# Kernel optimization log

Hardware: AMD Instinct MI355X
Metric: run time of the kernel (lower is better)

## Reference

```python
import jax, jax.numpy as jnp
from jax import lax
import numpy as np

H, W, C = 2160, 3840, 3
CROP = 3  # rows trimmed top and bottom before filtering


def median1d(x, size, axis):
    """Sliding-window median along `axis` with edge padding (matches
    np.pad(mode='edge') + centered window + np.median for odd size)."""
    pad = size // 2
    pw = [(0, 0)] * x.ndim
    pw[axis] = (pad, pad)
    xp = jnp.pad(x, pw, mode='edge')
    n = x.shape[axis]
    # stack the `size` shifted views -> (..., size), median = middle of sort
    windows = jnp.stack(
        [lax.slice_in_dim(xp, i, i + n, axis=axis) for i in range(size)], axis=-1)
    return jnp.sort(windows, axis=-1)[..., size // 2]


def shift1(x, axis):
    """np.pad(x,(1,0),'constant')[:-1] along `axis`: shift forward, zero-fill."""
    pw = [(0, 0)] * x.ndim
    pw[axis] = (1, 0)
    return lax.slice_in_dim(jnp.pad(x, pw), 0, x.shape[axis], axis=axis)


def setup_inputs() -> dict:
    key = jax.random.key(0)
    k1, k2 = jax.random.split(key)
    img = jax.random.normal(k1, (H, W, C), dtype=jnp.float32)
    mask = jax.random.randint(k2, (H, W), 0, 2, dtype=jnp.int32)
    return {"img": img, "mask": mask, "vertical_size": 5}


def reference(img, mask, vertical_size):
    # mask is read but unused by the original module's math.
    x = img[CROP:-CROP]                       # (H-6, W, C)
    # vertical pass: median(v), shift down 1, median(3) along rows
    v = median1d(x, vertical_size, axis=0)
    v = median1d(shift1(v, axis=0), 3, axis=0)
    # horizontal pass (original reuses vertical_size here): along columns
    h = median1d(v, vertical_size, axis=1)
    h = median1d(shift1(h, axis=1), 3, axis=1)
    return h
```

## Files before the change

### kernel.cpp

```cpp
#include <hip/hip_runtime.h>

#define HH    2160
#define WW    3840
#define CROPC 3
#define NN    (HH - 2*CROPC)
#define WFLAT (WW * 3)

constexpr int TY    = 16;
constexpr int TXF   = 192;
constexpr int SX    = TXF + 18;
constexpr int NTH   = 256;
constexpr int TPR   = 16;
constexpr int XROWS = TY + 6;

constexpr int PSTR  = 76;
constexpr int PLANE = TY * PSTR + 8;

__device__ __forceinline__ float vmed3(float a, float b, float c) {
    float r;
    asm("v_med3_f32 %0, %1, %2, %3" : "=v"(r) : "v"(a), "v"(b), "v"(c));
    return r;
}

__global__ __launch_bounds__(NTH, 8) void fused_median(const float* __restrict__ img,
                                                       float* __restrict__ out) {
    __shared__ float v2s[3 * PLANE];

    const int tid = threadIdx.x;
    const int r0 = blockIdx.y * TY;
    const int f0 = blockIdx.x * TXF;

    if (tid < SX) {
        const int ch   = tid % 3;
        const int pcol = tid / 3;
        const int cc   = min(max(f0 / 3 - 4 + pcol, 0), WW - 1);
        const float* colp = img + (size_t)CROPC * WFLAT + (cc * 3 + ch);

        float xv[XROWS];
        #pragma unroll
        for (int i = 0; i < XROWS; ++i) {
            const int rr = min(max(r0 - 4 + i, 0), NN - 1);
            xv[i] = colp[(size_t)rr * WFLAT];
        }
        asm volatile("" ::
            "v"(xv[0]),  "v"(xv[1]),  "v"(xv[2]),  "v"(xv[3]),  "v"(xv[4]),
            "v"(xv[5]),  "v"(xv[6]),  "v"(xv[7]),  "v"(xv[8]),  "v"(xv[9]),
            "v"(xv[10]), "v"(xv[11]), "v"(xv[12]), "v"(xv[13]), "v"(xv[14]),
            "v"(xv[15]), "v"(xv[16]), "v"(xv[17]), "v"(xv[18]), "v"(xv[19]),
            "v"(xv[20]), "v"(xv[21]));

        float lo0 = fminf(xv[0], xv[1]), hi0 = fmaxf(xv[0], xv[1]);
        float lo1 = fminf(xv[1], xv[2]), hi1 = fmaxf(xv[1], xv[2]);
        float vm2 = 0.f, vm1 = 0.f;
        #pragma unroll
        for (int s = 0; s < 18; ++s) {
            const float lo2 = fminf(xv[s+2], xv[s+3]);
            const float hi2 = fmaxf(xv[s+2], xv[s+3]);
            const float vc  = vmed3(xv[s+4], fmaxf(lo0, lo2), fminf(hi0, hi2));
            if (s >= 2) {
                const int rz = r0 + s - 2;
                float a = vm2, b = vm1;
                if (rz == NN - 1) a = b;
                if (rz == 1)      a = 0.f;
                if (rz == 0)    { a = 0.f; b = 0.f; }
                v2s[ch * PLANE + (s - 2) * PSTR + pcol] = vmed3(a, b, vc);
            }
            lo0 = lo1; hi0 = hi1; lo1 = lo2; hi1 = hi2;
            vm2 = vm1; vm1 = vc;
        }
    }
    __syncthreads();

    const int lr    = tid >> 4;
    const int kk    = tid & (TPR - 1);
    const int r_out = r0 + lr;
    if (r_out >= NN) return;

    const int cbase = f0 / 3 + 4 * kk;
    const bool edge = (cbase <= 1) || (cbase + 3 >= WW - 1);

    float o[12];
    #pragma unroll
    for (int c = 0; c < 3; ++c) {
        const float* pb = &v2s[c * PLANE + lr * PSTR + 4 * kk];
        const float4 q0 = *(const float4*)(pb);
        const float4 q1 = *(const float4*)(pb + 4);
        const float2 q2 = *(const float2*)(pb + 8);
        const float ss[10] = {q0.x,q0.y,q0.z,q0.w, q1.x,q1.y,q1.z,q1.w,
                              q2.x,q2.y};
        float plo[8], phi[8];
        #pragma unroll
        for (int i = 0; i < 8; ++i) {
            plo[i] = fminf(ss[i], ss[i+1]);
            phi[i] = fmaxf(ss[i], ss[i+1]);
        }
        float h[6];
        #pragma unroll
        for (int m = 0; m < 6; ++m)
            h[m] = vmed3(ss[m+4], fmaxf(plo[m], plo[m+2]), fminf(phi[m], phi[m+2]));
        if (!edge) {
            #pragma unroll
            for (int n = 0; n < 4; ++n)
                o[3*n + c] = vmed3(h[n], h[n+1], h[n+2]);
        } else {
            #pragma unroll
            for (int n = 0; n < 4; ++n) {
                const int ci = cbase + n;
                float A = h[n], B = h[n+1];
                if (ci == WW - 1) A = B;
                if (ci == 1)      A = 0.f;
                if (ci == 0)    { A = 0.f; B = 0.f; }
                o[3*n + c] = vmed3(A, B, h[n+2]);
            }
        }
    }

    float4* op = (float4*)(out + (size_t)r_out * WFLAT + f0 + 12 * kk);
    op[0] = make_float4(o[0], o[1], o[2],  o[3]);
    op[1] = make_float4(o[4], o[5], o[6],  o[7]);
    op[2] = make_float4(o[8], o[9], o[10], o[11]);
}

extern "C" void kernel_launch(void* const* d_in, const int* in_sizes, int n_in,
                              void* d_out, int out_size, void* d_ws, size_t ws_size,
                              hipStream_t stream) {
    const float* img = (const float*)d_in[0];
    float* out = (float*)d_out;
    dim3 grid(WFLAT / TXF, (NN + TY - 1) / TY);
    fused_median<<<grid, NTH, 0, stream>>>(img, out);
}
```

Before: 48.65 us.

## Replace shared-memory horizontal pass with wavefront shuffles, dropping the block barrier

The horizontal median passes now exchange neighbouring columns through cross-lane shuffles within each 64-lane wavefront, replacing the LDS staging buffer and the __syncthreads. Each wavefront computes 46 output floats and loads 18 halo lanes, so every thread does the vertical pass. Stores become scalar per-lane writes instead of float4 vectors. In exchange, about 28% of loaded columns are redundant halo, each row costs six shuffles, and stores are narrower.

```diff
diff --git a/kernel.cpp b/kernel.cpp
--- a/kernel.cpp
+++ b/kernel.cpp
@@ -7,118 +7,90 @@
 #define WFLAT (WW * 3)
 
 constexpr int TY    = 16;
-constexpr int TXF   = 192;
-constexpr int SX    = TXF + 18;
-constexpr int NTH   = 256;
-constexpr int TPR   = 16;
+constexpr int OPW   = 46;
+constexpr int WPB   = 4;
+constexpr int NTH   = 64 * WPB;
+constexpr int OPB   = OPW * WPB;
 constexpr int XROWS = TY + 6;
-
-constexpr int PSTR  = 76;
-constexpr int PLANE = TY * PSTR + 8;
 
 __device__ __forceinline__ float vmed3(float a, float b, float c) {
     float r;
     asm("v_med3_f32 %0, %1, %2, %3" : "=v"(r) : "v"(a), "v"(b), "v"(c));
     return r;
 }
+__device__ __forceinline__ float med5_7(float a, float b, float c, float d, float e) {
+    const float lo1 = fminf(a, b), hi1 = fmaxf(a, b);
+    const float lo2 = fminf(c, d), hi2 = fmaxf(c, d);
+    return vmed3(e, fmaxf(lo1, lo2), fminf(hi1, hi2));
+}
 
 __global__ __launch_bounds__(NTH, 8) void fused_median(const float* __restrict__ img,
                                                        float* __restrict__ out) {
-    __shared__ float v2s[3 * PLANE];
+    const int tid  = threadIdx.x;
+    const int lane = tid & 63;
+    const int wv   = tid >> 6;
+    const int r0   = blockIdx.y * TY;
+    const int fp12 = blockIdx.x * OPB + wv * OPW + lane;
+    const int fl   = fp12 - 12;
+    const int ch   = fp12 % 3;
+    const int cc   = min(max(fp12 / 3 - 4, 0), WW - 1);
+    const float* colp = img + (size_t)CROPC * WFLAT + (cc * 3 + ch);
 
-    const int tid = threadIdx.x;
-    const int r0 = blockIdx.y * TY;
-    const int f0 = blockIdx.x * TXF;
+    const int  ci       = fl / 3;
+    const bool store_ok = (lane >= 12) && (lane < 58) && (fl < WFLAT);
 
-    if (tid < SX) {
-        const int ch   = tid % 3;
-        const int pcol = tid / 3;
-        const int cc   = min(max(f0 / 3 - 4 + pcol, 0), WW - 1);
-        const float* colp = img + (size_t)CROPC * WFLAT + (cc * 3 + ch);
+    const int lm6 = max(lane - 6, 0), lm3 = max(lane - 3, 0);
+    const int lp3 = min(lane + 3, 63), lp6 = min(lane + 6, 63);
 
-        float xv[XROWS];
-        #pragma unroll
-        for (int i = 0; i < XROWS; ++i) {
-            const int rr = min(max(r0 - 4 + i, 0), NN - 1);
-            xv[i] = colp[(size_t)rr * WFLAT];
+    float xv[XROWS];
+    #pragma unroll
+    for (int i = 0; i < XROWS; ++i) {
+        const int rr = min(max(r0 - 4 + i, 0), NN - 1);
+        xv[i] = colp[(size_t)rr * WFLAT];
+    }
+    asm volatile("" ::
+        "v"(xv[0]),  "v"(xv[1]),  "v"(xv[2]),  "v"(xv[3]),  "v"(xv[4]),
+        "v"(xv[5]),  "v"(xv[6]),  "v"(xv[7]),  "v"(xv[8]),  "v"(xv[9]),
+        "v"(xv[10]), "v"(xv[11]), "v"(xv[12]), "v"(xv[13]), "v"(xv[14]),
+        "v"(xv[15]), "v"(xv[16]), "v"(xv[17]), "v"(xv[18]), "v"(xv[19]),
+        "v"(xv[20]), "v"(xv[21]));
+
+    float lo0 = fminf(xv[0], xv[1]), hi0 = fmaxf(xv[0], xv[1]);
+    float lo1 = fminf(xv[1], xv[2]), hi1 = fmaxf(xv[1], xv[2]);
+    float vm2 = 0.f, vm1 = 0.f;
+    #pragma unroll
+    for (int s = 0; s < TY + 2; ++s) {
+        const float lo2 = fminf(xv[s+2], xv[s+3]);
+        const float hi2 = fmaxf(xv[s+2], xv[s+3]);
+        const float vc  = vmed3(xv[s+4], fmaxf(lo0, lo2), fminf(hi0, hi2));
+        if (s >= 2) {
+            const int rz = r0 + s - 2;
+            float a = vm2, b = vm1;
+            if (rz == NN - 1) a = b;
+            if (rz == 1)      a = 0.f;
+            if (rz == 0)    { a = 0.f; b = 0.f; }
+            const float w = vmed3(a, b, vc);
+
+            const float m6 = __shfl(w, lm6, 64);
+            const float m3 = __shfl(w, lm3, 64);
+            const float p3 = __shfl(w, lp3, 64);
+            const float p6 = __shfl(w, lp6, 64);
+            const float h0 = med5_7(m6, m3, p3, p6, w);
+
+            const float hm3 = __shfl(h0, lm3, 64);
+            const float hm6 = __shfl(h0, lm6, 64);
+            float A = hm6, B = hm3;
+            if (ci == WW - 1) A = B;
+            if (ci == 1)      A = 0.f;
+            if (ci == 0)    { A = 0.f; B = 0.f; }
+            const float o = vmed3(A, B, h0);
+
+            if (store_ok && rz < NN)
+                out[(size_t)rz * WFLAT + fl] = o;
         }
-        asm volatile("" ::
-            "v"(xv[0]),  "v"(xv[1]),  "v"(xv[2]),  "v"(xv[3]),  "v"(xv[4]),
-            "v"(xv[5]),  "v"(xv[6]),  "v"(xv[7]),  "v"(xv[8]),  "v"(xv[9]),
-            "v"(xv[10]), "v"(xv[11]), "v"(xv[12]), "v"(xv[13]), "v"(xv[14]),
-            "v"(xv[15]), "v"(xv[16]), "v"(xv[17]), "v"(xv[18]), "v"(xv[19]),
-            "v"(xv[20]), "v"(xv[21]));
-
-        float lo0 = fminf(xv[0], xv[1]), hi0 = fmaxf(xv[0], xv[1]);
-        float lo1 = fminf(xv[1], xv[2]), hi1 = fmaxf(xv[1], xv[2]);
-        float vm2 = 0.f, vm1 = 0.f;
-        #pragma unroll
-        for (int s = 0; s < 18; ++s) {
-            const float lo2 = fminf(xv[s+2], xv[s+3]);
-            const float hi2 = fmaxf(xv[s+2], xv[s+3]);
-            const float vc  = vmed3(xv[s+4], fmaxf(lo0, lo2), fminf(hi0, hi2));
-            if (s >= 2) {
-                const int rz = r0 + s - 2;
-                float a = vm2, b = vm1;
-                if (rz == NN - 1) a = b;
-                if (rz == 1)      a = 0.f;
-                if (rz == 0)    { a = 0.f; b = 0.f; }
-                v2s[ch * PLANE + (s - 2) * PSTR + pcol] = vmed3(a, b, vc);
-            }
-            lo0 = lo1; hi0 = hi1; lo1 = lo2; hi1 = hi2;
-            vm2 = vm1; vm1 = vc;
-        }
+        lo0 = lo1; hi0 = hi1; lo1 = lo2; hi1 = hi2;
+        vm2 = vm1; vm1 = vc;
     }
-    __syncthreads();
-
-    const int lr    = tid >> 4;
-    const int kk    = tid & (TPR - 1);
-    const int r_out = r0 + lr;
-    if (r_out >= NN) return;
-
-    const int cbase = f0 / 3 + 4 * kk;
-    const bool edge = (cbase <= 1) || (cbase + 3 >= WW - 1);
-
-    float o[12];
-    #pragma unroll
-    for (int c = 0; c < 3; ++c) {
-        const float* pb = &v2s[c * PLANE + lr * PSTR + 4 * kk];
-        const float4 q0 = *(const float4*)(pb);
-        const float4 q1 = *(const float4*)(pb + 4);
-        const float2 q2 = *(const float2*)(pb + 8);
-        const float ss[10] = {q0.x,q0.y,q0.z,q0.w, q1.x,q1.y,q1.z,q1.w,
-                              q2.x,q2.y};
-        float plo[8], phi[8];
-        #pragma unroll
-        for (int i = 0; i < 8; ++i) {
-            plo[i] = fminf(ss[i], ss[i+1]);
-            phi[i] = fmaxf(ss[i], ss[i+1]);
-        }
-        float h[6];
-        #pragma unroll
-        for (int m = 0; m < 6; ++m)
-            h[m] = vmed3(ss[m+4], fmaxf(plo[m], plo[m+2]), fminf(phi[m], phi[m+2]));
-        if (!edge) {
-            #pragma unroll
-            for (int n = 0; n < 4; ++n)
-                o[3*n + c] = vmed3(h[n], h[n+1], h[n+2]);
-        } else {
-            #pragma unroll
-            for (int n = 0; n < 4; ++n) {
-                const int ci = cbase + n;
-                float A = h[n], B = h[n+1];
-                if (ci == WW - 1) A = B;
-                if (ci == 1)      A = 0.f;
-                if (ci == 0)    { A = 0.f; B = 0.f; }
-                o[3*n + c] = vmed3(A, B, h[n+2]);
-            }
-        }
-    }
-
-    float4* op = (float4*)(out + (size_t)r_out * WFLAT + f0 + 12 * kk);
-    op[0] = make_float4(o[0], o[1], o[2],  o[3]);
-    op[1] = make_float4(o[4], o[5], o[6],  o[7]);
-    op[2] = make_float4(o[8], o[9], o[10], o[11]);
 }
 
 extern "C" void kernel_launch(void* const* d_in, const int* in_sizes, int n_in,
@@ -126,6 +98,7 @@
                               hipStream_t stream) {
     const float* img = (const float*)d_in[0];
     float* out = (float*)d_out;
-    dim3 grid(WFLAT / TXF, (NN + TY - 1) / TY);
+    dim3 grid((WFLAT + OPB - 1) / OPB,
+              (NN + TY - 1) / TY);
     fused_median<<<grid, NTH, 0, stream>>>(img, out);
 }
```

New measurement: 48.78 us. About the same (+0.3%).
